# Optimization experiments

Hardware: AMD Instinct MI355X
Metric: run time of the kernel (lower is better)

The kernel has to match this reference:

```python
import jax, jax.numpy as jnp
import numpy as np

DIM = 768
HEADS = 12
HEAD_DIM = DIM // HEADS
HIDDEN = int(DIM * 1.0)  # mlp_ratio = 1.0
EPS = 1e-5


def layer_norm(x, g, b):
    mu = jnp.mean(x, axis=-1, keepdims=True)
    var = jnp.mean(jnp.square(x - mu), axis=-1, keepdims=True)
    return (x - mu) * jax.lax.rsqrt(var + EPS) * g + b


def setup_inputs() -> dict:
    key = jax.random.key(0)
    ks = jax.random.split(key, 8)
    s = 0.02
    return {
        "x": jax.random.normal(ks[0], (8, 1024, DIM), dtype=jnp.float32),
        "mask": jnp.ones((8, 1024), dtype=jnp.int32),
        "g1": jnp.ones((DIM,), jnp.float32),
        "b1": jnp.zeros((DIM,), jnp.float32),
        "w_qkv": jax.random.normal(ks[1], (DIM, 3 * DIM), jnp.float32) * s,
        "w_proj": jax.random.normal(ks[2], (DIM, DIM), jnp.float32) * s,
        "b_proj": jnp.zeros((DIM,), jnp.float32),
        "g2": jnp.ones((DIM,), jnp.float32),
        "b2": jnp.zeros((DIM,), jnp.float32),
        "w_fc1": jax.random.normal(ks[3], (DIM, HIDDEN), jnp.float32) * s,
        "b_fc1": jnp.zeros((HIDDEN,), jnp.float32),
        "w_fc2": jax.random.normal(ks[4], (HIDDEN, DIM), jnp.float32) * s,
        "b_fc2": jnp.zeros((DIM,), jnp.float32),
    }


def reference(x, mask, g1, b1, w_qkv, w_proj, b_proj, g2, b2, w_fc1, b_fc1, w_fc2, b_fc2):
    B, N, C = x.shape
    scale = HEAD_DIM ** -0.5

    # --- attention (pre-norm) ---
    h = layer_norm(x, g1, b1)
    qkv = (h @ w_qkv).reshape(B, N, 3, HEADS, HEAD_DIM)
    qkv = jnp.transpose(qkv, (2, 0, 3, 1, 4))  # 3, b, h, n, d
    q, k, v = qkv[0], qkv[1], qkv[2]

    attn = jnp.einsum("bhnd,bhmd->bhnm", q, k) * scale
    # mask: (B, N) -> pairwise mask (B, 1, N, N)
    pair = (mask[:, None, :, None] * mask[:, None, None, :]) != 0
    attn = jnp.where(pair, attn, jnp.float32(-1e9))
    attn = jax.nn.softmax(attn, axis=-1)

    o = jnp.einsum("bhnm,bhmd->bhnd", attn, v)
    o = jnp.transpose(o, (0, 2, 1, 3)).reshape(B, N, C)
    o = o @ w_proj + b_proj
    x = x + o

    # --- MLP (pre-norm) ---
    h2 = layer_norm(x, g2, b2)
    h2 = jax.nn.gelu(h2 @ w_fc1 + b_fc1, approximate=False)
    h2 = h2 @ w_fc2 + b_fc2
    return x + h2
```

## Files before the change

kernel.cpp:

```cpp
#include <hip/hip_runtime.h>
#include <stdint.h>
#include <math.h>

using short8 = __attribute__((ext_vector_type(8))) short;
using f32x4  = __attribute__((ext_vector_type(4))) float;

#define DEV __device__ __forceinline__
#define S_VMCNT(n) asm volatile("s_waitcnt vmcnt(" #n ")" ::: "memory")
#define S_LGKM0()  asm volatile("s_waitcnt lgkmcnt(0)" ::: "memory")
#define SCHED0()   __builtin_amdgcn_sched_barrier(0)
#define SBAR()     __builtin_amdgcn_s_barrier()

DEV unsigned short f2bf(float f) {
    union { float f; unsigned u; } c; c.f = f;
    unsigned u = c.u;
    unsigned r = (u + 0x7FFFu + ((u >> 16) & 1u)) >> 16;
    return (unsigned short)r;
}

DEV float bf2f(unsigned short h) {
    union { unsigned u; float f; } c; c.u = ((unsigned)h) << 16;
    return c.f;
}

DEV void gld16(const unsigned short* g, unsigned short* l) {
    __builtin_amdgcn_global_load_lds(
        (const __attribute__((address_space(1))) void*)g,
        (__attribute__((address_space(3))) void*)l, 16, 0, 0);
}

DEV unsigned ldsaddr(unsigned short* p) {
    return (unsigned)(uintptr_t)(__attribute__((address_space(3))) unsigned short*)p;
}

DEV unsigned cvtpk(float lo, float hi) {
    unsigned r;
    asm("v_cvt_pk_bf16_f32 %0, %1, %2" : "=v"(r) : "v"(lo), "v"(hi));
    return r;
}

DEV uint2 tr16(unsigned addr) {
    uint2 r;
    asm volatile("ds_read_b64_tr_b16 %0, %1" : "=v"(r) : "v"(addr));
    return r;
}

__global__ __launch_bounds__(256) void k_transpose_all(
    const float* __restrict__ w0, const float* __restrict__ w1,
    const float* __restrict__ w2, const float* __restrict__ w3,
    unsigned short* __restrict__ o0, unsigned short* __restrict__ o1,
    unsigned short* __restrict__ o2, unsigned short* __restrict__ o3)
{
    __shared__ float tile[32][33];
    int z = blockIdx.z;
    const float* W = (z == 0) ? w0 : (z == 1) ? w1 : (z == 2) ? w2 : w3;
    unsigned short* Wt = (z == 0) ? o0 : (z == 1) ? o1 : (z == 2) ? o2 : o3;
    int N = (z == 0) ? 2304 : 768;
    int n0 = blockIdx.x * 32, k0 = blockIdx.y * 32;
    if (n0 >= N) return;
    int tx = threadIdx.x, ty = threadIdx.y;
#pragma unroll
    for (int i = 0; i < 4; i++) {
        int k = k0 + ty + i * 8;
        tile[ty + i * 8][tx] = W[(size_t)k * N + n0 + tx];
    }
    __syncthreads();
#pragma unroll
    for (int i = 0; i < 4; i++) {
        int n = n0 + ty + i * 8;
        Wt[(size_t)n * 768 + k0 + tx] = f2bf(tile[tx][ty + i * 8]);
    }
}

template<int BF>
__global__ __launch_bounds__(256) void k_layernorm(
    const void* __restrict__ xin, const float* __restrict__ g,
    const float* __restrict__ b, unsigned short* __restrict__ out)
{
    int row = blockIdx.x;
    int tid = threadIdx.x;
    float v0, v1, v2;
    if (BF) {
        const unsigned short* xr = (const unsigned short*)xin + (size_t)row * 768;
        v0 = bf2f(xr[tid]); v1 = bf2f(xr[tid + 256]); v2 = bf2f(xr[tid + 512]);
    } else {
        const float* xr = (const float*)xin + (size_t)row * 768;
        v0 = xr[tid]; v1 = xr[tid + 256]; v2 = xr[tid + 512];
    }
    float s1 = v0 + v1 + v2;
    float s2 = v0 * v0 + v1 * v1 + v2 * v2;
#pragma unroll
    for (int off = 32; off >= 1; off >>= 1) {
        s1 += __shfl_down(s1, off);
        s2 += __shfl_down(s2, off);
    }
    __shared__ float red[8];
    int wid = tid >> 6, lane = tid & 63;
    if (lane == 0) { red[wid] = s1; red[4 + wid] = s2; }
    __syncthreads();
    s1 = red[0] + red[1] + red[2] + red[3];
    s2 = red[4] + red[5] + red[6] + red[7];
    float mu = s1 * (1.0f / 768.0f);
    float var = s2 * (1.0f / 768.0f) - mu * mu;
    float rs = rsqrtf(var + 1e-5f);
    unsigned short* orow = out + (size_t)row * 768;
    orow[tid]       = f2bf((v0 - mu) * rs * g[tid]       + b[tid]);
    orow[tid + 256] = f2bf((v1 - mu) * rs * g[tid + 256] + b[tid + 256]);
    orow[tid + 512] = f2bf((v2 - mu) * rs * g[tid + 512] + b[tid + 512]);
}

template<int EPI, int BN>
__global__ __launch_bounds__(256) void k_gemm(
    const unsigned short* __restrict__ A, const unsigned short* __restrict__ Bt,
    const float* __restrict__ bias,
    const float* __restrict__ residF, const unsigned short* __restrict__ residH,
    float* __restrict__ outF, unsigned short* __restrict__ outH,
    unsigned short* __restrict__ qb, unsigned short* __restrict__ kb,
    unsigned short* __restrict__ vtb)
{
    constexpr int KK = 768, NK = 12;
    constexpr int MI = (BN == 128) ? 4 : 2;
    constexpr int NJ = 4;
    __shared__ __align__(16) unsigned short As[2][128 * 64];
    __shared__ __align__(16) unsigned short Bs[2][BN * 64];

    int tid = threadIdx.x;
    int lane = tid & 63, wid = tid >> 6;

    int gy = gridDim.y;
    int nwg = 64 * gy;
    int bid = blockIdx.x + blockIdx.y * 64;
    int nid = (bid & 7) * (nwg >> 3) + (bid >> 3);
    int bx = nid / gy;
    int by = nid - bx * gy;
    int m0 = bx * 128, n0 = by * BN;

    int wr = (BN == 128) ? (wid >> 1) * 64 : wid * 32;
    int wc = (BN == 128) ? (wid & 1) * 64 : 0;
    int fr = lane & 15, fg = lane >> 4;
    int fr7 = fr & 7;

    f32x4 zero4 = {0.f, 0.f, 0.f, 0.f};
    f32x4 acc[MI][NJ];
#pragma unroll
    for (int mi = 0; mi < MI; mi++)
#pragma unroll
        for (int nj = 0; nj < NJ; nj++) acc[mi][nj] = zero4;

    int srow = wid * 8 + (lane >> 3);
    int schk = (lane & 7) ^ (lane >> 3);
    const unsigned short* ga = A  + (size_t)(m0 + srow) * KK + schk * 8;
    const unsigned short* gb = Bt + (size_t)(n0 + srow) * KK + schk * 8;

    auto stage = [&](int kt, int s) {
        int ko = kt * 64;
#pragma unroll
        for (int i = 0; i < 4; i++)
            gld16(ga + (size_t)i * 32 * KK + ko, As[s] + i * 2048 + wid * 512);
#pragma unroll
        for (int i = 0; i < BN / 32; i++)
            gld16(gb + (size_t)i * 32 * KK + ko, Bs[s] + i * 2048 + wid * 512);
    };

    int aoff0 = (wr + fr) * 64;
    int boff0 = (wc + fr) * 64;

    stage(0, 0);

    for (int k = 0; k < NK; ++k) {
        if (k + 1 < NK) {
            stage(k + 1, (k + 1) & 1);
            if constexpr (BN == 128) { S_VMCNT(8); } else { S_VMCNT(6); }
        } else {
            S_VMCNT(0);
        }
        SCHED0(); SBAR(); SCHED0();

        const unsigned short* Ac = As[k & 1];
        const unsigned short* Bc = Bs[k & 1];
#pragma unroll
        for (int kk = 0; kk < 2; ++kk) {
            int off = (((kk << 2) | fg) ^ fr7) * 8;
            short8 af[MI], bfv[NJ];
#pragma unroll
            for (int mi = 0; mi < MI; mi++)
                af[mi] = *(const short8*)(Ac + aoff0 + mi * 1024 + off);
#pragma unroll
            for (int nj = 0; nj < NJ; nj++)
                bfv[nj] = *(const short8*)(Bc + boff0 + nj * 1024 + off);
#pragma unroll
            for (int mi = 0; mi < MI; mi++)
#pragma unroll
                for (int nj = 0; nj < NJ; nj++)
                    acc[mi][nj] = __builtin_amdgcn_mfma_f32_16x16x32_bf16(
                        af[mi], bfv[nj], acc[mi][nj], 0, 0, 0);
        }
        SCHED0(); SBAR(); SCHED0();
    }

#pragma unroll
    for (int mi = 0; mi < MI; mi++) {
#pragma unroll
        for (int nj = 0; nj < NJ; nj++) {
#pragma unroll
            for (int i = 0; i < 4; i++) {
                int grow = m0 + wr + mi * 16 + fg * 4 + i;
                int gcol = n0 + wc + nj * 16 + fr;
                float v = acc[mi][nj][i];
                if (EPI == 0) {
                    int part = gcol / 768;
                    int wi = gcol - part * 768;
                    int head = wi >> 6, d = wi & 63;
                    int bb = grow >> 10, n = grow & 1023;
                    size_t base = ((size_t)(bb * 12 + head)) << 16;
                    unsigned short bv = f2bf(v);
                    if (part == 0)      qb[base + (size_t)n * 64 + d] = bv;
                    else if (part == 1) kb[base + (size_t)n * 64 + d] = bv;
                    else                vtb[base + (size_t)d * 1024 + n] = bv;
                } else if (EPI == 1) {
                    size_t idx = (size_t)grow * 768 + gcol;
                    outH[idx] = f2bf(v + bias[gcol] + residF[idx]);
                } else if (EPI == 2) {
                    float t = v + bias[gcol];
                    outH[(size_t)grow * 768 + gcol] =
                        f2bf(0.5f * t * (1.0f + erff(t * 0.70710678118f)));
                } else {
                    size_t idx = (size_t)grow * 768 + gcol;
                    outF[idx] = v + bias[gcol] + bf2f(residH[idx]);
                }
            }
        }
    }
}

__global__ __launch_bounds__(256) void k_attn(
    const unsigned short* __restrict__ Q, const unsigned short* __restrict__ Kk,
    const unsigned short* __restrict__ Vt, const int* __restrict__ mask,
    unsigned short* __restrict__ O)
{
    __shared__ __align__(16) unsigned short Ks[2][64 * 64];
    __shared__ __align__(16) unsigned short Vs[2][64 * 64];
    __shared__ __align__(16) unsigned short PT[4][64 * 16];
    __shared__ float mskf[1024];

    int tid = threadIdx.x, lane = tid & 63, wid = tid >> 6;
    int bid = blockIdx.x + blockIdx.y * 16;
    int nid = (bid & 7) * 192 + (bid >> 3);
    int qt = nid & 15;
    int bh = nid >> 4;
    int b = bh / 12;
    int hh = bh - b * 12;
    int fr = lane & 15, fg = lane >> 4;

    const unsigned short* qg = Q  + ((size_t)bh << 16);
    const unsigned short* kg = Kk + ((size_t)bh << 16);
    const unsigned short* vg = Vt + ((size_t)bh << 16);

    for (int i = tid; i < 1024; i += 256)
        mskf[i] = mask[b * 1024 + i] ? 1.f : 0.f;

    short8 qf[2];
    {
        const unsigned short* qp = qg + (size_t)(qt * 64 + wid * 16 + fr) * 64 + fg * 8;
        qf[0] = *(const short8*)(qp);
        qf[1] = *(const short8*)(qp + 32);
    }

    int srow = wid * 8 + (lane >> 3);
    int schk = (lane & 7) ^ ((lane >> 3) & 7);
    const unsigned short* kgp = kg + (size_t)srow * 64 + schk * 8;
    const unsigned short* vgp = vg + (size_t)srow * 1024 + schk * 8;

    auto stage = [&](int kn, int s) {
        gld16(kgp + (size_t)(kn * 64) * 64, Ks[s] + wid * 512);
        gld16(kgp + (size_t)(kn * 64 + 32) * 64, Ks[s] + wid * 512 + 2048);
        gld16(vgp + kn * 64, Vs[s] + wid * 512);
        gld16(vgp + 32 * 1024 + kn * 64, Vs[s] + wid * 512 + 2048);
    };

    stage(0, 0);
    __syncthreads();

    f32x4 zero4 = {0.f, 0.f, 0.f, 0.f};
    f32x4 oacc[4];
    f32x4 lacc = zero4;
#pragma unroll
    for (int df = 0; df < 4; df++) oacc[df] = zero4;

    short8 ones8;
#pragma unroll
    for (int j = 0; j < 8; j++) ones8[j] = (short)0x3F80;

    const float SC = 0.125f * 1.44269504f;

    unsigned ptb = ldsaddr(&PT[wid][0]);
    unsigned trbase = ptb + fg * 8 * 32 + fr * 2;
    unsigned short* pw = &PT[wid][0];

    int cur = 0;
    for (int kc = 0; kc < 16; ++kc) {
        if (kc < 15) {
            stage(kc + 1, cur ^ 1);
            S_VMCNT(4);
        } else {
            S_VMCNT(0);
        }
        SCHED0(); SBAR(); SCHED0();

        f32x4 s[4];
        int pos0 = fg ^ (fr & 7);
        int pos1 = (fg + 4) ^ (fr & 7);
        __builtin_amdgcn_s_setprio(1);
#pragma unroll
        for (int nf = 0; nf < 4; ++nf) {
            int row = nf * 16 + fr;
            short8 b0 = *(const short8*)(Ks[cur] + row * 64 + pos0 * 8);
            short8 b1 = *(const short8*)(Ks[cur] + row * 64 + pos1 * 8);
            f32x4 a = zero4;
            a = __builtin_amdgcn_mfma_f32_16x16x32_bf16(qf[0], b0, a, 0, 0, 0);
            a = __builtin_amdgcn_mfma_f32_16x16x32_bf16(qf[1], b1, a, 0, 0, 0);
            s[nf] = a;
        }
        __builtin_amdgcn_s_setprio(0);

#pragma unroll
        for (int nf = 0; nf < 4; nf++) {
            float mk = mskf[kc * 64 + nf * 16 + fr];
            float p0 = __builtin_amdgcn_exp2f(s[nf][0] * SC) * mk;
            float p1 = __builtin_amdgcn_exp2f(s[nf][1] * SC) * mk;
            float p2 = __builtin_amdgcn_exp2f(s[nf][2] * SC) * mk;
            float p3 = __builtin_amdgcn_exp2f(s[nf][3] * SC) * mk;
            uint2 w; w.x = cvtpk(p0, p1); w.y = cvtpk(p2, p3);
            *(uint2*)(pw + (nf * 16 + fr) * 16 + fg * 4) = w;
        }
        S_LGKM0();
        SCHED0();

        uint2 r00 = tr16(trbase);
        uint2 r01 = tr16(trbase + 128);
        uint2 r10 = tr16(trbase + 1024);
        uint2 r11 = tr16(trbase + 1024 + 128);
        S_LGKM0();
        SCHED0();

        union { unsigned u[4]; short8 s8; } pa0, pa1;
        pa0.u[0] = r00.x; pa0.u[1] = r00.y; pa0.u[2] = r01.x; pa0.u[3] = r01.y;
        pa1.u[0] = r10.x; pa1.u[1] = r10.y; pa1.u[2] = r11.x; pa1.u[3] = r11.y;

        __builtin_amdgcn_s_setprio(1);
#pragma unroll
        for (int df = 0; df < 4; df++) {
            int rv = df * 16 + fr;
            int posv0 = fg ^ (fr & 7);
            int posv1 = (4 + fg) ^ (fr & 7);
            short8 vb0 = *(const short8*)(Vs[cur] + rv * 64 + posv0 * 8);
            short8 vb1 = *(const short8*)(Vs[cur] + rv * 64 + posv1 * 8);
            oacc[df] = __builtin_amdgcn_mfma_f32_16x16x32_bf16(pa0.s8, vb0, oacc[df], 0, 0, 0);
            oacc[df] = __builtin_amdgcn_mfma_f32_16x16x32_bf16(pa1.s8, vb1, oacc[df], 0, 0, 0);
        }
        lacc = __builtin_amdgcn_mfma_f32_16x16x32_bf16(pa0.s8, ones8, lacc, 0, 0, 0);
        lacc = __builtin_amdgcn_mfma_f32_16x16x32_bf16(pa1.s8, ones8, lacc, 0, 0, 0);
        __builtin_amdgcn_s_setprio(0);

        S_LGKM0();
        SCHED0(); SBAR(); SCHED0();
        cur ^= 1;
    }

#pragma unroll
    for (int i = 0; i < 4; i++) {
        float inv = 1.0f / fmaxf(lacc[i], 1e-30f);
        size_t rowbase = ((size_t)(b * 1024 + qt * 64 + wid * 16 + fg * 4 + i)) * 768
                         + hh * 64 + fr;
#pragma unroll
        for (int df = 0; df < 4; df++)
            O[rowbase + df * 16] = f2bf(oacc[df][i] * inv);
    }
}

extern "C" void kernel_launch(void* const* d_in, const int* in_sizes, int n_in,
                              void* d_out, int out_size, void* d_ws, size_t ws_size,
                              hipStream_t stream)
{
    const float* x      = (const float*)d_in[0];
    const int*   mask   = (const int*)d_in[1];
    const float* g1     = (const float*)d_in[2];
    const float* b1     = (const float*)d_in[3];
    const float* w_qkv  = (const float*)d_in[4];
    const float* w_proj = (const float*)d_in[5];
    const float* b_proj = (const float*)d_in[6];
    const float* g2     = (const float*)d_in[7];
    const float* b2     = (const float*)d_in[8];
    const float* w_fc1  = (const float*)d_in[9];
    const float* b_fc1  = (const float*)d_in[10];
    const float* w_fc2  = (const float*)d_in[11];
    const float* b_fc2  = (const float*)d_in[12];
    float* out = (float*)d_out;

    char* ws = (char*)d_ws;
    unsigned short* wqkv_t  = (unsigned short*)(ws + 0);
    unsigned short* wproj_t = (unsigned short*)(ws + 3538944);
    unsigned short* wfc1_t  = (unsigned short*)(ws + 4718592);
    unsigned short* wfc2_t  = (unsigned short*)(ws + 5898240);
    unsigned short* bufA    = (unsigned short*)(ws + 7077888);
    unsigned short* bufB    = (unsigned short*)(ws + 19660800);
    unsigned short* qb      = (unsigned short*)(ws + 32243712);
    unsigned short* kb      = (unsigned short*)(ws + 44826624);
    unsigned short* vtb     = (unsigned short*)(ws + 57409536);
    unsigned short* x1b     = (unsigned short*)(ws + 69992448);

    k_transpose_all<<<dim3(72, 24, 4), dim3(32, 8), 0, stream>>>(
        w_qkv, w_proj, w_fc1, w_fc2, wqkv_t, wproj_t, wfc1_t, wfc2_t);

    k_layernorm<0><<<8192, 256, 0, stream>>>(x, g1, b1, bufA);

    k_gemm<0, 128><<<dim3(64, 18), 256, 0, stream>>>(bufA, wqkv_t,
        nullptr, nullptr, nullptr, nullptr, nullptr, qb, kb, vtb);

    k_attn<<<dim3(16, 96), 256, 0, stream>>>(qb, kb, vtb, mask, bufB);

    k_gemm<1, 64><<<dim3(64, 12), 256, 0, stream>>>(bufB, wproj_t,
        b_proj, x, nullptr, nullptr, x1b, nullptr, nullptr, nullptr);

    k_layernorm<1><<<8192, 256, 0, stream>>>(x1b, g2, b2, bufA);

    k_gemm<2, 64><<<dim3(64, 12), 256, 0, stream>>>(bufA, wfc1_t,
        b_fc1, nullptr, nullptr, nullptr, bufB, nullptr, nullptr, nullptr);

    k_gemm<3, 64><<<dim3(64, 12), 256, 0, stream>>>(bufB, wfc2_t,
        b_fc2, nullptr, x1b, out, nullptr, nullptr, nullptr, nullptr);
}
```

Baseline: 188.2 us.

## Deepen GEMM and attention pipelines with multi-buffered LDS and software-pipelined softmax

The GEMM now uses a 32-wide K tile with four LDS stages and prefetches two tiles ahead. This drops the trailing barrier per iteration and changes the swizzle to match. The attention kernel triple-buffers K/V and double-buffers the P tile so that the PV MMA for the previous chunk overlaps the QK MMA and softmax of the current one. The aim is to hide load and exp latency behind MFMA work, at the cost of more LDS, more registers, and more complex buffer rotation and barrier logic.

```diff
diff --git a/kernel.cpp b/kernel.cpp
--- a/kernel.cpp
+++ b/kernel.cpp
@@ -118,11 +118,11 @@
     unsigned short* __restrict__ qb, unsigned short* __restrict__ kb,
     unsigned short* __restrict__ vtb)
 {
-    constexpr int KK = 768, NK = 12;
+    constexpr int KK = 768, NK = 24;
     constexpr int MI = (BN == 128) ? 4 : 2;
     constexpr int NJ = 4;
-    __shared__ __align__(16) unsigned short As[2][128 * 64];
-    __shared__ __align__(16) unsigned short Bs[2][BN * 64];
+    __shared__ __align__(16) unsigned short As[4][128 * 32];
+    __shared__ __align__(16) unsigned short Bs[4][BN * 32];
 
     int tid = threadIdx.x;
     int lane = tid & 63, wid = tid >> 6;
@@ -138,7 +138,6 @@
     int wr = (BN == 128) ? (wid >> 1) * 64 : wid * 32;
     int wc = (BN == 128) ? (wid & 1) * 64 : 0;
     int fr = lane & 15, fg = lane >> 4;
-    int fr7 = fr & 7;
 
     f32x4 zero4 = {0.f, 0.f, 0.f, 0.f};
     f32x4 acc[MI][NJ];
@@ -147,55 +146,51 @@
 #pragma unroll
         for (int nj = 0; nj < NJ; nj++) acc[mi][nj] = zero4;
 
-    int srow = wid * 8 + (lane >> 3);
-    int schk = (lane & 7) ^ (lane >> 3);
-    const unsigned short* ga = A  + (size_t)(m0 + srow) * KK + schk * 8;
+    int srow = tid >> 2;
+    int schk = (tid & 3) ^ ((tid >> 3) & 3);
+    const unsigned short* ga = A + (size_t)(m0 + srow) * KK + schk * 8;
     const unsigned short* gb = Bt + (size_t)(n0 + srow) * KK + schk * 8;
 
     auto stage = [&](int kt, int s) {
-        int ko = kt * 64;
-#pragma unroll
-        for (int i = 0; i < 4; i++)
-            gld16(ga + (size_t)i * 32 * KK + ko, As[s] + i * 2048 + wid * 512);
-#pragma unroll
-        for (int i = 0; i < BN / 32; i++)
-            gld16(gb + (size_t)i * 32 * KK + ko, Bs[s] + i * 2048 + wid * 512);
+        int ko = kt * 32;
+        gld16(ga + ko, As[s] + wid * 512);
+        gld16(ga + (size_t)64 * KK + ko, As[s] + 2048 + wid * 512);
+        gld16(gb + ko, Bs[s] + wid * 512);
+        if (BN == 128) gld16(gb + (size_t)64 * KK + ko, Bs[s] + 2048 + wid * 512);
     };
 
-    int aoff0 = (wr + fr) * 64;
-    int boff0 = (wc + fr) * 64;
+    int rsw = (fg ^ ((fr >> 1) & 3)) * 8;
+    int abase = (wr + fr) * 32 + rsw;
+    int bbase = (wc + fr) * 32 + rsw;
 
     stage(0, 0);
+    stage(1, 1);
 
     for (int k = 0; k < NK; ++k) {
-        if (k + 1 < NK) {
-            stage(k + 1, (k + 1) & 1);
+        if (k + 2 < NK) {
+            stage(k + 2, (k + 2) & 3);
+            SCHED0();
             if constexpr (BN == 128) { S_VMCNT(8); } else { S_VMCNT(6); }
+        } else if (k + 1 < NK) {
+            if constexpr (BN == 128) { S_VMCNT(4); } else { S_VMCNT(3); }
         } else {
             S_VMCNT(0);
         }
         SCHED0(); SBAR(); SCHED0();
 
-        const unsigned short* Ac = As[k & 1];
-        const unsigned short* Bc = Bs[k & 1];
-#pragma unroll
-        for (int kk = 0; kk < 2; ++kk) {
-            int off = (((kk << 2) | fg) ^ fr7) * 8;
-            short8 af[MI], bfv[NJ];
-#pragma unroll
-            for (int mi = 0; mi < MI; mi++)
-                af[mi] = *(const short8*)(Ac + aoff0 + mi * 1024 + off);
+        const unsigned short* Ac = As[k & 3];
+        const unsigned short* Bc = Bs[k & 3];
+        short8 af[MI], bfv[NJ];
+#pragma unroll
+        for (int mi = 0; mi < MI; mi++) af[mi]  = *(const short8*)(Ac + abase + mi * 512);
+#pragma unroll
+        for (int nj = 0; nj < NJ; nj++) bfv[nj] = *(const short8*)(Bc + bbase + nj * 512);
+#pragma unroll
+        for (int mi = 0; mi < MI; mi++)
 #pragma unroll
             for (int nj = 0; nj < NJ; nj++)
-                bfv[nj] = *(const short8*)(Bc + boff0 + nj * 1024 + off);
-#pragma unroll
-            for (int mi = 0; mi < MI; mi++)
-#pragma unroll
-                for (int nj = 0; nj < NJ; nj++)
-                    acc[mi][nj] = __builtin_amdgcn_mfma_f32_16x16x32_bf16(
-                        af[mi], bfv[nj], acc[mi][nj], 0, 0, 0);
-        }
-        SCHED0(); SBAR(); SCHED0();
+                acc[mi][nj] = __builtin_amdgcn_mfma_f32_16x16x32_bf16(
+                    af[mi], bfv[nj], acc[mi][nj], 0, 0, 0);
     }
 
 #pragma unroll
@@ -238,9 +233,9 @@
     const unsigned short* __restrict__ Vt, const int* __restrict__ mask,
     unsigned short* __restrict__ O)
 {
-    __shared__ __align__(16) unsigned short Ks[2][64 * 64];
-    __shared__ __align__(16) unsigned short Vs[2][64 * 64];
-    __shared__ __align__(16) unsigned short PT[4][64 * 16];
+    __shared__ __align__(16) unsigned short KsA[3 * 4096];
+    __shared__ __align__(16) unsigned short VsA[3 * 4096];
+    __shared__ __align__(16) unsigned short PTA[4 * 2 * 1024];
     __shared__ float mskf[1024];
 
     int tid = threadIdx.x, lane = tid & 63, wid = tid >> 6;
@@ -272,10 +267,12 @@
     const unsigned short* vgp = vg + (size_t)srow * 1024 + schk * 8;
 
     auto stage = [&](int kn, int s) {
-        gld16(kgp + (size_t)(kn * 64) * 64, Ks[s] + wid * 512);
-        gld16(kgp + (size_t)(kn * 64 + 32) * 64, Ks[s] + wid * 512 + 2048);
-        gld16(vgp + kn * 64, Vs[s] + wid * 512);
-        gld16(vgp + 32 * 1024 + kn * 64, Vs[s] + wid * 512 + 2048);
+        unsigned short* Kd = &KsA[s * 4096];
+        unsigned short* Vd = &VsA[s * 4096];
+        gld16(kgp + (size_t)(kn * 64) * 64, Kd + wid * 512);
+        gld16(kgp + (size_t)(kn * 64 + 32) * 64, Kd + wid * 512 + 2048);
+        gld16(vgp + kn * 64, Vd + wid * 512);
+        gld16(vgp + 32 * 1024 + kn * 64, Vd + wid * 512 + 2048);
     };
 
     stage(0, 0);
@@ -293,36 +290,102 @@
 
     const float SC = 0.125f * 1.44269504f;
 
-    unsigned ptb = ldsaddr(&PT[wid][0]);
-    unsigned trbase = ptb + fg * 8 * 32 + fr * 2;
-    unsigned short* pw = &PT[wid][0];
-
-    int cur = 0;
-    for (int kc = 0; kc < 16; ++kc) {
-        if (kc < 15) {
-            stage(kc + 1, cur ^ 1);
-            S_VMCNT(4);
-        } else {
-            S_VMCNT(0);
-        }
+    unsigned short* pwave = &PTA[wid * 2048];
+    unsigned ptw = ldsaddr(pwave);
+    unsigned trofs = fg * 256 + fr * 2;
+
+    int pos0 = fg ^ (fr & 7);
+    int pos1 = (fg + 4) ^ (fr & 7);
+
+    {
+        stage(1, 1);
+        S_VMCNT(4);
         SCHED0(); SBAR(); SCHED0();
-
+        const unsigned short* Kc = &KsA[0];
         f32x4 s[4];
-        int pos0 = fg ^ (fr & 7);
-        int pos1 = (fg + 4) ^ (fr & 7);
         __builtin_amdgcn_s_setprio(1);
 #pragma unroll
         for (int nf = 0; nf < 4; ++nf) {
             int row = nf * 16 + fr;
-            short8 b0 = *(const short8*)(Ks[cur] + row * 64 + pos0 * 8);
-            short8 b1 = *(const short8*)(Ks[cur] + row * 64 + pos1 * 8);
+            short8 b0 = *(const short8*)(Kc + row * 64 + pos0 * 8);
+            short8 b1 = *(const short8*)(Kc + row * 64 + pos1 * 8);
             f32x4 a = zero4;
             a = __builtin_amdgcn_mfma_f32_16x16x32_bf16(qf[0], b0, a, 0, 0, 0);
             a = __builtin_amdgcn_mfma_f32_16x16x32_bf16(qf[1], b1, a, 0, 0, 0);
             s[nf] = a;
         }
         __builtin_amdgcn_s_setprio(0);
-
+#pragma unroll
+        for (int nf = 0; nf < 4; nf++) {
+            float mk = mskf[nf * 16 + fr];
+            float p0 = __builtin_amdgcn_exp2f(s[nf][0] * SC) * mk;
+            float p1 = __builtin_amdgcn_exp2f(s[nf][1] * SC) * mk;
+            float p2 = __builtin_amdgcn_exp2f(s[nf][2] * SC) * mk;
+            float p3 = __builtin_amdgcn_exp2f(s[nf][3] * SC) * mk;
+            uint2 w; w.x = cvtpk(p0, p1); w.y = cvtpk(p2, p3);
+            *(uint2*)(pwave + (nf * 16 + fr) * 16 + fg * 4) = w;
+        }
+        SBAR();
+    }
+
+    int pp = 1;
+    int pb = 0, cb = 1, sb = 2;
+    for (int kc = 1; kc < 16; ++kc) {
+        if (kc < 15) {
+            stage(kc + 1, sb);
+            SCHED0();
+            S_VMCNT(4);
+        } else {
+            S_VMCNT(0);
+        }
+        SCHED0(); SBAR(); SCHED0();
+
+        const unsigned short* Kc = &KsA[cb * 4096];
+        const unsigned short* Vp = &VsA[pb * 4096];
+
+        short8 kb0[4], kb1[4], vb0[4], vb1[4];
+#pragma unroll
+        for (int nf = 0; nf < 4; ++nf) {
+            int row = nf * 16 + fr;
+            kb0[nf] = *(const short8*)(Kc + row * 64 + pos0 * 8);
+            kb1[nf] = *(const short8*)(Kc + row * 64 + pos1 * 8);
+        }
+        unsigned trb = ptw + (pp ^ 1) * 2048 + trofs;
+        uint2 r00 = tr16(trb);
+        uint2 r01 = tr16(trb + 128);
+        uint2 r10 = tr16(trb + 1024);
+        uint2 r11 = tr16(trb + 1024 + 128);
+#pragma unroll
+        for (int df = 0; df < 4; ++df) {
+            int rv = df * 16 + fr;
+            vb0[df] = *(const short8*)(Vp + rv * 64 + pos0 * 8);
+            vb1[df] = *(const short8*)(Vp + rv * 64 + pos1 * 8);
+        }
+        S_LGKM0(); SCHED0();
+
+        union { unsigned u[4]; short8 s8; } pa0, pa1;
+        pa0.u[0] = r00.x; pa0.u[1] = r00.y; pa0.u[2] = r01.x; pa0.u[3] = r01.y;
+        pa1.u[0] = r10.x; pa1.u[1] = r10.y; pa1.u[2] = r11.x; pa1.u[3] = r11.y;
+
+        f32x4 s[4];
+        __builtin_amdgcn_s_setprio(1);
+#pragma unroll
+        for (int nf = 0; nf < 4; ++nf) {
+            f32x4 a = zero4;
+            a = __builtin_amdgcn_mfma_f32_16x16x32_bf16(qf[0], kb0[nf], a, 0, 0, 0);
+            a = __builtin_amdgcn_mfma_f32_16x16x32_bf16(qf[1], kb1[nf], a, 0, 0, 0);
+            s[nf] = a;
+        }
+#pragma unroll
+        for (int df = 0; df < 4; df++) {
+            oacc[df] = __builtin_amdgcn_mfma_f32_16x16x32_bf16(pa0.s8, vb0[df], oacc[df], 0, 0, 0);
+            oacc[df] = __builtin_amdgcn_mfma_f32_16x16x32_bf16(pa1.s8, vb1[df], oacc[df], 0, 0, 0);
+        }
+        lacc = __builtin_amdgcn_mfma_f32_16x16x32_bf16(pa0.s8, ones8, lacc, 0, 0, 0);
+        lacc = __builtin_amdgcn_mfma_f32_16x16x32_bf16(pa1.s8, ones8, lacc, 0, 0, 0);
+        __builtin_amdgcn_s_setprio(0);
+
+        unsigned short* pw = pwave + pp * 1024;
 #pragma unroll
         for (int nf = 0; nf < 4; nf++) {
             float mk = mskf[kc * 64 + nf * 16 + fr];
@@ -333,38 +396,37 @@
             uint2 w; w.x = cvtpk(p0, p1); w.y = cvtpk(p2, p3);
             *(uint2*)(pw + (nf * 16 + fr) * 16 + fg * 4) = w;
         }
-        S_LGKM0();
-        SCHED0();
-
-        uint2 r00 = tr16(trbase);
-        uint2 r01 = tr16(trbase + 128);
-        uint2 r10 = tr16(trbase + 1024);
-        uint2 r11 = tr16(trbase + 1024 + 128);
-        S_LGKM0();
-        SCHED0();
-
+        SBAR();
+
+        int t = pb; pb = cb; cb = sb; sb = t;
+        pp ^= 1;
+    }
+
+    {
+        const unsigned short* Vp = &VsA[0];
+        unsigned trb = ptw + (pp ^ 1) * 2048 + trofs;
+        uint2 r00 = tr16(trb);
+        uint2 r01 = tr16(trb + 128);
+        uint2 r10 = tr16(trb + 1024);
+        uint2 r11 = tr16(trb + 1024 + 128);
+        short8 vb0[4], vb1[4];
+#pragma unroll
+        for (int df = 0; df < 4; ++df) {
+            int rv = df * 16 + fr;
+            vb0[df] = *(const short8*)(Vp + rv * 64 + pos0 * 8);
+            vb1[df] = *(const short8*)(Vp + rv * 64 + pos1 * 8);
+        }
+        S_LGKM0(); SCHED0();
         union { unsigned u[4]; short8 s8; } pa0, pa1;
         pa0.u[0] = r00.x; pa0.u[1] = r00.y; pa0.u[2] = r01.x; pa0.u[3] = r01.y;
         pa1.u[0] = r10.x; pa1.u[1] = r10.y; pa1.u[2] = r11.x; pa1.u[3] = r11.y;
-
-        __builtin_amdgcn_s_setprio(1);
 #pragma unroll
         for (int df = 0; df < 4; df++) {
-            int rv = df * 16 + fr;
-            int posv0 = fg ^ (fr & 7);
-            int posv1 = (4 + fg) ^ (fr & 7);
-            short8 vb0 = *(const short8*)(Vs[cur] + rv * 64 + posv0 * 8);
-            short8 vb1 = *(const short8*)(Vs[cur] + rv * 64 + posv1 * 8);
-            oacc[df] = __builtin_amdgcn_mfma_f32_16x16x32_bf16(pa0.s8, vb0, oacc[df], 0, 0, 0);
-            oacc[df] = __builtin_amdgcn_mfma_f32_16x16x32_bf16(pa1.s8, vb1, oacc[df], 0, 0, 0);
+            oacc[df] = __builtin_amdgcn_mfma_f32_16x16x32_bf16(pa0.s8, vb0[df], oacc[df], 0, 0, 0);
+            oacc[df] = __builtin_amdgcn_mfma_f32_16x16x32_bf16(pa1.s8, vb1[df], oacc[df], 0, 0, 0);
         }
         lacc = __builtin_amdgcn_mfma_f32_16x16x32_bf16(pa0.s8, ones8, lacc, 0, 0, 0);
         lacc = __builtin_amdgcn_mfma_f32_16x16x32_bf16(pa1.s8, ones8, lacc, 0, 0, 0);
-        __builtin_amdgcn_s_setprio(0);
-
-        S_LGKM0();
-        SCHED0(); SBAR(); SCHED0();
-        cur ^= 1;
     }
 
 #pragma unroll
```

Result: slower. 218.2 us (+15.9%).

## Software-pipeline attention with 512-thread blocks and triple-buffered K/V

Applied to the files above, without the earlier changes.

The attention kernel now runs 8 waves per block over 128 query rows, so each K/V tile staged in LDS is shared by twice as many waves. K/V buffering goes from double to triple. The loop is software-pipelined so the QK^T MFMAs and exp work for tile kc overlap the PV MFMAs for tile kc-1, with partial lgkmcnt waits replacing full drains. This aims to hide LDS and exp latency and halve per-block K/V traffic, at the cost of more registers, a larger LDS footprint that may reduce occupancy, and fewer blocks in the grid.

```diff
diff --git a/kernel.cpp b/kernel.cpp
--- a/kernel.cpp
+++ b/kernel.cpp
@@ -7,6 +7,7 @@
 
 #define DEV __device__ __forceinline__
 #define S_VMCNT(n) asm volatile("s_waitcnt vmcnt(" #n ")" ::: "memory")
+#define S_LGKM(n)  asm volatile("s_waitcnt lgkmcnt(" #n ")" ::: "memory")
 #define S_LGKM0()  asm volatile("s_waitcnt lgkmcnt(0)" ::: "memory")
 #define SCHED0()   __builtin_amdgcn_sched_barrier(0)
 #define SBAR()     __builtin_amdgcn_s_barrier()
@@ -233,21 +234,21 @@
     }
 }
 
-__global__ __launch_bounds__(256) void k_attn(
+__global__ __launch_bounds__(512) void k_attn(
     const unsigned short* __restrict__ Q, const unsigned short* __restrict__ Kk,
     const unsigned short* __restrict__ Vt, const int* __restrict__ mask,
     unsigned short* __restrict__ O)
 {
-    __shared__ __align__(16) unsigned short Ks[2][64 * 64];
-    __shared__ __align__(16) unsigned short Vs[2][64 * 64];
-    __shared__ __align__(16) unsigned short PT[4][64 * 16];
+    __shared__ __align__(16) unsigned short KsA[3 * 4096];
+    __shared__ __align__(16) unsigned short VsA[3 * 4096];
+    __shared__ __align__(16) unsigned short PT[8 * 1024];
     __shared__ float mskf[1024];
 
     int tid = threadIdx.x, lane = tid & 63, wid = tid >> 6;
-    int bid = blockIdx.x + blockIdx.y * 16;
-    int nid = (bid & 7) * 192 + (bid >> 3);
-    int qt = nid & 15;
-    int bh = nid >> 4;
+    int bid = blockIdx.x + blockIdx.y * 8;
+    int nid = (bid & 7) * 96 + (bid >> 3);
+    int qt = nid & 7;
+    int bh = nid >> 3;
     int b = bh / 12;
     int hh = bh - b * 12;
     int fr = lane & 15, fg = lane >> 4;
@@ -256,12 +257,12 @@
     const unsigned short* kg = Kk + ((size_t)bh << 16);
     const unsigned short* vg = Vt + ((size_t)bh << 16);
 
-    for (int i = tid; i < 1024; i += 256)
+    for (int i = tid; i < 1024; i += 512)
         mskf[i] = mask[b * 1024 + i] ? 1.f : 0.f;
 
     short8 qf[2];
     {
-        const unsigned short* qp = qg + (size_t)(qt * 64 + wid * 16 + fr) * 64 + fg * 8;
+        const unsigned short* qp = qg + (size_t)(qt * 128 + wid * 16 + fr) * 64 + fg * 8;
         qf[0] = *(const short8*)(qp);
         qf[1] = *(const short8*)(qp + 32);
     }
@@ -272,10 +273,8 @@
     const unsigned short* vgp = vg + (size_t)srow * 1024 + schk * 8;
 
     auto stage = [&](int kn, int s) {
-        gld16(kgp + (size_t)(kn * 64) * 64, Ks[s] + wid * 512);
-        gld16(kgp + (size_t)(kn * 64 + 32) * 64, Ks[s] + wid * 512 + 2048);
-        gld16(vgp + kn * 64, Vs[s] + wid * 512);
-        gld16(vgp + 32 * 1024 + kn * 64, Vs[s] + wid * 512 + 2048);
+        gld16(kgp + (size_t)(kn * 64) * 64, &KsA[s * 4096] + wid * 512);
+        gld16(vgp + kn * 64, &VsA[s * 4096] + wid * 512);
     };
 
     stage(0, 0);
@@ -293,84 +292,141 @@
 
     const float SC = 0.125f * 1.44269504f;
 
-    unsigned ptb = ldsaddr(&PT[wid][0]);
-    unsigned trbase = ptb + fg * 8 * 32 + fr * 2;
-    unsigned short* pw = &PT[wid][0];
-
-    int cur = 0;
+    unsigned short* pw = &PT[wid * 1024];
+    unsigned trbase = ldsaddr(pw) + fg * 256 + fr * 2;
+
+    int pos0 = fg ^ (fr & 7);
+    int pos1 = (fg + 4) ^ (fr & 7);
+
+#pragma unroll
     for (int kc = 0; kc < 16; ++kc) {
-        if (kc < 15) {
-            stage(kc + 1, cur ^ 1);
-            S_VMCNT(4);
-        } else {
-            S_VMCNT(0);
-        }
+        S_VMCNT(0);
         SCHED0(); SBAR(); SCHED0();
-
-        f32x4 s[4];
-        int pos0 = fg ^ (fr & 7);
-        int pos1 = (fg + 4) ^ (fr & 7);
-        __builtin_amdgcn_s_setprio(1);
+        if (kc < 15) { stage(kc + 1, (kc + 1) % 3); SCHED0(); }
+
+        const unsigned short* Kc = &KsA[(kc % 3) * 4096];
+        short8 kb0[4], kb1[4];
 #pragma unroll
         for (int nf = 0; nf < 4; ++nf) {
             int row = nf * 16 + fr;
-            short8 b0 = *(const short8*)(Ks[cur] + row * 64 + pos0 * 8);
-            short8 b1 = *(const short8*)(Ks[cur] + row * 64 + pos1 * 8);
-            f32x4 a = zero4;
-            a = __builtin_amdgcn_mfma_f32_16x16x32_bf16(qf[0], b0, a, 0, 0, 0);
-            a = __builtin_amdgcn_mfma_f32_16x16x32_bf16(qf[1], b1, a, 0, 0, 0);
-            s[nf] = a;
-        }
-        __builtin_amdgcn_s_setprio(0);
-
-#pragma unroll
-        for (int nf = 0; nf < 4; nf++) {
-            float mk = mskf[kc * 64 + nf * 16 + fr];
-            float p0 = __builtin_amdgcn_exp2f(s[nf][0] * SC) * mk;
-            float p1 = __builtin_amdgcn_exp2f(s[nf][1] * SC) * mk;
-            float p2 = __builtin_amdgcn_exp2f(s[nf][2] * SC) * mk;
-            float p3 = __builtin_amdgcn_exp2f(s[nf][3] * SC) * mk;
-            uint2 w; w.x = cvtpk(p0, p1); w.y = cvtpk(p2, p3);
-            *(uint2*)(pw + (nf * 16 + fr) * 16 + fg * 4) = w;
-        }
-        S_LGKM0();
+            kb0[nf] = *(const short8*)(Kc + row * 64 + pos0 * 8);
+            kb1[nf] = *(const short8*)(Kc + row * 64 + pos1 * 8);
+        }
         SCHED0();
 
+        f32x4 s[4];
+        if (kc > 0) {
+            S_LGKM(8);
+            uint2 r00 = tr16(trbase);
+            uint2 r01 = tr16(trbase + 128);
+            uint2 r10 = tr16(trbase + 1024);
+            uint2 r11 = tr16(trbase + 1024 + 128);
+            S_LGKM(4);
+            SCHED0();
+            __builtin_amdgcn_s_setprio(1);
+#pragma unroll
+            for (int nf = 0; nf < 4; ++nf) {
+                f32x4 a = zero4;
+                a = __builtin_amdgcn_mfma_f32_16x16x32_bf16(qf[0], kb0[nf], a, 0, 0, 0);
+                a = __builtin_amdgcn_mfma_f32_16x16x32_bf16(qf[1], kb1[nf], a, 0, 0, 0);
+                s[nf] = a;
+            }
+            __builtin_amdgcn_s_setprio(0);
+
+            const unsigned short* Vp = &VsA[(((kc - 1) % 3)) * 4096];
+            short8 vb0[4], vb1[4];
+#pragma unroll
+            for (int df = 0; df < 4; ++df) {
+                int rv = df * 16 + fr;
+                vb0[df] = *(const short8*)(Vp + rv * 64 + pos0 * 8);
+                vb1[df] = *(const short8*)(Vp + rv * 64 + pos1 * 8);
+            }
+
+            union { unsigned u[4]; short8 s8; } pa0, pa1;
+            pa0.u[0] = r00.x; pa0.u[1] = r00.y; pa0.u[2] = r01.x; pa0.u[3] = r01.y;
+            pa1.u[0] = r10.x; pa1.u[1] = r10.y; pa1.u[2] = r11.x; pa1.u[3] = r11.y;
+
+            uint2 w[4];
+#pragma unroll
+            for (int nf = 0; nf < 4; nf++) {
+                float mk = mskf[kc * 64 + nf * 16 + fr];
+                float p0 = __builtin_amdgcn_exp2f(s[nf][0] * SC) * mk;
+                float p1 = __builtin_amdgcn_exp2f(s[nf][1] * SC) * mk;
+                float p2 = __builtin_amdgcn_exp2f(s[nf][2] * SC) * mk;
+                float p3 = __builtin_amdgcn_exp2f(s[nf][3] * SC) * mk;
+                w[nf].x = cvtpk(p0, p1); w[nf].y = cvtpk(p2, p3);
+            }
+
+            S_LGKM0();
+            SCHED0();
+            __builtin_amdgcn_s_setprio(1);
+#pragma unroll
+            for (int df = 0; df < 4; df++) {
+                oacc[df] = __builtin_amdgcn_mfma_f32_16x16x32_bf16(pa0.s8, vb0[df], oacc[df], 0, 0, 0);
+                oacc[df] = __builtin_amdgcn_mfma_f32_16x16x32_bf16(pa1.s8, vb1[df], oacc[df], 0, 0, 0);
+            }
+            lacc = __builtin_amdgcn_mfma_f32_16x16x32_bf16(pa0.s8, ones8, lacc, 0, 0, 0);
+            lacc = __builtin_amdgcn_mfma_f32_16x16x32_bf16(pa1.s8, ones8, lacc, 0, 0, 0);
+            __builtin_amdgcn_s_setprio(0);
+
+#pragma unroll
+            for (int nf = 0; nf < 4; nf++)
+                *(uint2*)(pw + (nf * 16 + fr) * 16 + fg * 4) = w[nf];
+        } else {
+            S_LGKM0();
+            SCHED0();
+            __builtin_amdgcn_s_setprio(1);
+#pragma unroll
+            for (int nf = 0; nf < 4; ++nf) {
+                f32x4 a = zero4;
+                a = __builtin_amdgcn_mfma_f32_16x16x32_bf16(qf[0], kb0[nf], a, 0, 0, 0);
+                a = __builtin_amdgcn_mfma_f32_16x16x32_bf16(qf[1], kb1[nf], a, 0, 0, 0);
+                s[nf] = a;
+            }
+            __builtin_amdgcn_s_setprio(0);
+#pragma unroll
+            for (int nf = 0; nf < 4; nf++) {
+                float mk = mskf[nf * 16 + fr];
+                float p0 = __builtin_amdgcn_exp2f(s[nf][0] * SC) * mk;
+                float p1 = __builtin_amdgcn_exp2f(s[nf][1] * SC) * mk;
+                float p2 = __builtin_amdgcn_exp2f(s[nf][2] * SC) * mk;
+                float p3 = __builtin_amdgcn_exp2f(s[nf][3] * SC) * mk;
+                uint2 w0; w0.x = cvtpk(p0, p1); w0.y = cvtpk(p2, p3);
+                *(uint2*)(pw + (nf * 16 + fr) * 16 + fg * 4) = w0;
+            }
+        }
+    }
+
+    {
         uint2 r00 = tr16(trbase);
         uint2 r01 = tr16(trbase + 128);
         uint2 r10 = tr16(trbase + 1024);
         uint2 r11 = tr16(trbase + 1024 + 128);
-        S_LGKM0();
-        SCHED0();
-
+        const unsigned short* Vp = &VsA[0];
+        short8 vb0[4], vb1[4];
+#pragma unroll
+        for (int df = 0; df < 4; ++df) {
+            int rv = df * 16 + fr;
+            vb0[df] = *(const short8*)(Vp + rv * 64 + pos0 * 8);
+            vb1[df] = *(const short8*)(Vp + rv * 64 + pos1 * 8);
+        }
+        S_LGKM0(); SCHED0();
         union { unsigned u[4]; short8 s8; } pa0, pa1;
         pa0.u[0] = r00.x; pa0.u[1] = r00.y; pa0.u[2] = r01.x; pa0.u[3] = r01.y;
         pa1.u[0] = r10.x; pa1.u[1] = r10.y; pa1.u[2] = r11.x; pa1.u[3] = r11.y;
-
-        __builtin_amdgcn_s_setprio(1);
 #pragma unroll
         for (int df = 0; df < 4; df++) {
-            int rv = df * 16 + fr;
-            int posv0 = fg ^ (fr & 7);
-            int posv1 = (4 + fg) ^ (fr & 7);
-            short8 vb0 = *(const short8*)(Vs[cur] + rv * 64 + posv0 * 8);
-            short8 vb1 = *(const short8*)(Vs[cur] + rv * 64 + posv1 * 8);
-            oacc[df] = __builtin_amdgcn_mfma_f32_16x16x32_bf16(pa0.s8, vb0, oacc[df], 0, 0, 0);
-            oacc[df] = __builtin_amdgcn_mfma_f32_16x16x32_bf16(pa1.s8, vb1, oacc[df], 0, 0, 0);
+            oacc[df] = __builtin_amdgcn_mfma_f32_16x16x32_bf16(pa0.s8, vb0[df], oacc[df], 0, 0, 0);
+            oacc[df] = __builtin_amdgcn_mfma_f32_16x16x32_bf16(pa1.s8, vb1[df], oacc[df], 0, 0, 0);
         }
         lacc = __builtin_amdgcn_mfma_f32_16x16x32_bf16(pa0.s8, ones8, lacc, 0, 0, 0);
         lacc = __builtin_amdgcn_mfma_f32_16x16x32_bf16(pa1.s8, ones8, lacc, 0, 0, 0);
-        __builtin_amdgcn_s_setprio(0);
-
-        S_LGKM0();
-        SCHED0(); SBAR(); SCHED0();
-        cur ^= 1;
     }
 
 #pragma unroll
     for (int i = 0; i < 4; i++) {
         float inv = 1.0f / fmaxf(lacc[i], 1e-30f);
-        size_t rowbase = ((size_t)(b * 1024 + qt * 64 + wid * 16 + fg * 4 + i)) * 768
+        size_t rowbase = ((size_t)(b * 1024 + qt * 128 + wid * 16 + fg * 4 + i)) * 768
                          + hh * 64 + fr;
 #pragma unroll
         for (int df = 0; df < 4; df++)
@@ -417,7 +473,7 @@
     k_gemm<0, 128><<<dim3(64, 18), 256, 0, stream>>>(bufA, wqkv_t,
         nullptr, nullptr, nullptr, nullptr, nullptr, qb, kb, vtb);
 
-    k_attn<<<dim3(16, 96), 256, 0, stream>>>(qb, kb, vtb, mask, bufB);
+    k_attn<<<dim3(8, 96), 512, 0, stream>>>(qb, kb, vtb, mask, bufB);
 
     k_gemm<1, 64><<<dim3(64, 12), 256, 0, stream>>>(bufB, wproj_t,
         b_proj, x, nullptr, nullptr, x1b, nullptr, nullptr, nullptr);
```

Result: faster. 176.8 us (-6.1%).
